# Kernel tuning notes

Hardware: AMD Instinct MI355X
Metric: run time of the kernel (lower is better)

The kernel has to match this reference:

```python
import jax, jax.numpy as jnp
import numpy as np

B, S, D = 8, 2048, 1024
D_FF = 1024  # FeedForward default d_ff
EPS = 1e-5   # nn.LayerNorm default


def layernorm(x, g, b):
    mu = jnp.mean(x, axis=-1, keepdims=True)
    var = jnp.mean(jnp.square(x - mu), axis=-1, keepdims=True)
    return (x - mu) * jax.lax.rsqrt(var + EPS) * g + b


def setup_inputs() -> dict:
    key = jax.random.key(0)
    ks = jax.random.split(key, 12)
    s = 1.0 / np.sqrt(D)
    return {
        "x": jax.random.normal(ks[0], (B, S, D), jnp.float32),
        "mask": jax.random.randint(ks[1], (B, S), 0, 2, jnp.int32),
        "ln1_g": jnp.ones((D,), jnp.float32),
        "ln1_b": jnp.zeros((D,), jnp.float32),
        "Wq": jax.random.normal(ks[2], (D, D), jnp.float32) * s,
        "bq": jnp.zeros((D,), jnp.float32),
        "Wk": jax.random.normal(ks[3], (D, D), jnp.float32) * s,
        "bk": jnp.zeros((D,), jnp.float32),
        "Wo": jax.random.normal(ks[4], (D, D), jnp.float32) * s,
        "bo": jnp.zeros((D,), jnp.float32),
        "ln2_g": jnp.ones((D,), jnp.float32),
        "ln2_b": jnp.zeros((D,), jnp.float32),
        "W1": jax.random.normal(ks[5], (D, D_FF), jnp.float32) * s,
        "b1": jnp.zeros((D_FF,), jnp.float32),
        "W2": jax.random.normal(ks[6], (D_FF, D), jnp.float32) * (1.0 / np.sqrt(D_FF)),
        "b2": jnp.zeros((D,), jnp.float32),
    }


def reference(x, mask, ln1_g, ln1_b, Wq, bq, Wk, bk, Wo, bo, ln2_g, ln2_b, W1, b1, W2, b2):
    # pre-norm
    xn = layernorm(x, ln1_g, ln1_b)
    q = xn @ Wq + bq
    k = xn @ Wk + bk
    v = xn @ Wk + bk  # faithful bug: original uses k_linear for v
    scores = jnp.einsum('bqd,bkd->bqk', q, k) / np.sqrt(D)
    scores = jnp.where(mask[:, None, :] == 0, jnp.float32(-1e9), scores)
    w = jax.nn.softmax(scores, axis=-1)
    attn = jnp.einsum('bqk,bkd->bqd', w, v) @ Wo + bo
    x2 = x + attn  # dropout identity (eval)
    xn2 = layernorm(x2, ln2_g, ln2_b)
    ff = jax.nn.relu(xn2 @ W1 + b1) @ W2 + b2
    out = x2 + ff
    return (out, w)
```

## Files before the change

kernel.cpp:

```cpp
#include <hip/hip_runtime.h>
#include <cstdint>
#include <cstddef>

#define BB 8
#define SS 2048
#define DD 1024

typedef unsigned short bf16_t;
typedef __attribute__((ext_vector_type(8))) short bf16x8;
typedef __attribute__((ext_vector_type(4))) float f32x4;
typedef __attribute__((ext_vector_type(4))) short short4v;

#define EPI_BF16   0
#define EPI_SCORES 1
#define EPI_RESID  2

__device__ __forceinline__ bf16_t f2bf(float f) {
  union { float f; unsigned u; } v; v.f = f;
  unsigned r = v.u + 0x7FFFu + ((v.u >> 16) & 1u);
  return (bf16_t)(r >> 16);
}

__device__ __forceinline__ void async_copy16(const void* g, void* l) {
  auto gp = reinterpret_cast<unsigned int __attribute__((address_space(1)))*>(
      reinterpret_cast<uintptr_t>(g));
  auto lp = reinterpret_cast<unsigned int __attribute__((address_space(3)))*>(
      reinterpret_cast<uintptr_t>(l));
  __builtin_amdgcn_global_load_lds(gp, lp, 16, 0, 0);
}

#define MM(i, j, Af, Bf) \
  acc[i][j] = __builtin_amdgcn_mfma_f32_16x16x32_bf16(Af, Bf, acc[i][j], 0, 0, 0)

#define LDA8(D, MH)                                                        \
  { const char* Ah_ = ldsc + (D) * 65536 + (MH) * 16384;                   \
    aF[0] = *(const bf16x8*)(Ah_ + aro +    0 + s0);                       \
    aF[1] = *(const bf16x8*)(Ah_ + aro + 2048 + s0);                       \
    aF[2] = *(const bf16x8*)(Ah_ + aro + 4096 + s0);                       \
    aF[3] = *(const bf16x8*)(Ah_ + aro + 6144 + s0);                       \
    aF[4] = *(const bf16x8*)(Ah_ + aro +    0 + s1);                       \
    aF[5] = *(const bf16x8*)(Ah_ + aro + 2048 + s1);                       \
    aF[6] = *(const bf16x8*)(Ah_ + aro + 4096 + s1);                       \
    aF[7] = *(const bf16x8*)(Ah_ + aro + 6144 + s1); }

#define LDB4(D, NH, BF)                                                    \
  { const char* Bh_ = ldsc + (D) * 65536 + 32768 + (NH) * 16384;           \
    BF[0] = *(const bf16x8*)(Bh_ + bro +    0 + s0);                       \
    BF[1] = *(const bf16x8*)(Bh_ + bro + 2048 + s0);                       \
    BF[2] = *(const bf16x8*)(Bh_ + bro +    0 + s1);                       \
    BF[3] = *(const bf16x8*)(Bh_ + bro + 2048 + s1); }

#define MFMA16(MH, NH, BF)                                                 \
  __builtin_amdgcn_s_setprio(1);                                           \
  MM((MH)*4+0,(NH)*2+0,aF[0],BF[0]); MM((MH)*4+1,(NH)*2+0,aF[1],BF[0]);    \
  MM((MH)*4+2,(NH)*2+0,aF[2],BF[0]); MM((MH)*4+3,(NH)*2+0,aF[3],BF[0]);    \
  MM((MH)*4+0,(NH)*2+1,aF[0],BF[1]); MM((MH)*4+1,(NH)*2+1,aF[1],BF[1]);    \
  MM((MH)*4+2,(NH)*2+1,aF[2],BF[1]); MM((MH)*4+3,(NH)*2+1,aF[3],BF[1]);    \
  MM((MH)*4+0,(NH)*2+0,aF[4],BF[2]); MM((MH)*4+1,(NH)*2+0,aF[5],BF[2]);    \
  MM((MH)*4+2,(NH)*2+0,aF[6],BF[2]); MM((MH)*4+3,(NH)*2+0,aF[7],BF[2]);    \
  MM((MH)*4+0,(NH)*2+1,aF[4],BF[3]); MM((MH)*4+1,(NH)*2+1,aF[5],BF[3]);    \
  MM((MH)*4+2,(NH)*2+1,aF[6],BF[3]); MM((MH)*4+3,(NH)*2+1,aF[7],BF[3]);    \
  __builtin_amdgcn_s_setprio(0);

template <int EPI, bool RELU>
__global__ __launch_bounds__(512, 2)
void gemm256(const bf16_t* __restrict__ A, const bf16_t* __restrict__ BT,
             void* __restrict__ Cv,
             const float* __restrict__ bias,
             const float* __restrict__ bias2,
             const float* __restrict__ resid,
             const int* __restrict__ mask,
             int Mt, int Nt, int Z, int nchunk,
             int K, int lda, int ldb, int ldc,
             long long sA, long long sB, long long sC, long long sMask,
             float scale)
{
  __shared__ __align__(16) bf16_t lds_[65536];
  char* ldsc = (char*)lds_;

  const int b = blockIdx.x;
  const int Cchunk = (Z * Mt * Nt) >> 3;
  int idx = (b & 7) * Cchunk + (b >> 3);
  const int per_z = Mt * Nt;
  const int z = idx / per_z;  idx -= z * per_z;
  const int per_nc = Mt * nchunk;
  const int nc = idx / per_nc; idx -= nc * per_nc;
  const int mt = idx / nchunk;
  const int nin = idx - mt * nchunk;
  const int m0 = mt * 256;
  const int n0 = (nc * nchunk + nin) * 256;

  const int tid  = threadIdx.x;
  const int wave = tid >> 6;
  const int lane = tid & 63;
  const int wr   = wave >> 2, wc = wave & 3;
  const int lr   = lane & 15, quad = lane >> 4;

  const bf16_t* Ab = A  + (size_t)z * (size_t)sA;
  const bf16_t* Bb = BT + (size_t)z * (size_t)sB;

  f32x4 acc[8][4];
#pragma unroll
  for (int i = 0; i < 8; ++i)
#pragma unroll
    for (int j = 0; j < 4; ++j)
#pragma unroll
      for (int r = 0; r < 4; ++r) acc[i][j][r] = 0.0f;

  const bf16_t* gA[2]; const bf16_t* gB[2]; char* lA[2]; char* lB[2];
#pragma unroll
  for (int u = 0; u < 2; ++u) {
    const int c = tid + u * 512;
    const int rl = c >> 3;
    const int csw = (((c & 7) ^ (rl & 7)) << 3);
    const int rowA = ((rl & 64) << 1) + (rl & 63);
    const int rowB = ((rl & 96) << 1) + (rl & 31);
    gA[u] = Ab + (size_t)(m0 + rowA) * lda + csw;
    gB[u] = Bb + (size_t)(n0 + rowB) * ldb + csw;
    lA[u] = ldsc + c * 16;
    lB[u] = ldsc + 32768 + c * 16;
  }
  const int ldA64 = lda << 6, ldB64 = ldb << 5;

  auto stageA = [&](int d, int mh, int kt) {
    const int go = mh * ldA64 + kt;
    const int lo = d * 65536 + mh * 16384;
#pragma unroll
    for (int u = 0; u < 2; ++u) async_copy16(gA[u] + go, lA[u] + lo);
  };
  auto stageB = [&](int d, int nh, int kt) {
    const int go = nh * ldB64 + kt;
    const int lo = d * 65536 + nh * 16384;
#pragma unroll
    for (int u = 0; u < 2; ++u) async_copy16(gB[u] + go, lB[u] + lo);
  };

  const int s0  = ((quad ^ (lr & 7)) << 4);
  const int s1  = s0 ^ 64;
  const int aro = (wr * 64 + lr) << 7;
  const int bro = (wc * 32 + lr) << 7;

  bf16x8 aF[8];
  bf16x8 bF0[4], bF1[4];

  const int NT = K >> 6;

  stageA(0, 0, 0); stageA(0, 1, 0); stageB(0, 0, 0); stageB(0, 1, 0);
  if (NT > 1) {
    stageA(1, 0, 64); stageB(1, 0, 64);
    asm volatile("s_waitcnt vmcnt(4)" ::: "memory");
  } else {
    asm volatile("s_waitcnt vmcnt(0)" ::: "memory");
  }
  __builtin_amdgcn_s_barrier();

#pragma unroll 2
  for (int t = 0; t < NT; ++t) {
    const int d  = t & 1;
    const int k1 = (t + 1) << 6;
    const int k2 = (t + 2) << 6;

    LDA8(d, 0); LDB4(d, 0, bF0);
    if (t + 1 < NT) stageA(d ^ 1, 1, k1);
    __builtin_amdgcn_s_barrier();
    MFMA16(0, 0, bF0);

    LDB4(d, 1, bF1);
    if (t + 1 < NT) stageB(d ^ 1, 1, k1);
    __builtin_amdgcn_s_barrier();
    MFMA16(0, 1, bF1);

    LDA8(d, 1);
    if (t + 2 < NT) stageA(d, 0, k2);
    __builtin_amdgcn_s_barrier();
    MFMA16(1, 1, bF1);

    if (t + 2 < NT) {
      stageB(d, 0, k2);
      asm volatile("s_waitcnt vmcnt(4)" ::: "memory");
    } else {
      asm volatile("s_waitcnt vmcnt(0)" ::: "memory");
    }
    __builtin_amdgcn_s_barrier();
    MFMA16(1, 0, bF0);
  }

#pragma unroll
  for (int i = 0; i < 8; ++i) {
    const int gmb = m0 + wr * 128 + (i >> 2) * 64 + (i & 3) * 16 + quad * 4;
#pragma unroll
    for (int j = 0; j < 4; ++j) {
      const int gn = n0 + wc * 64 + (j >> 1) * 32 + (j & 1) * 16 + lr;
      float bv = 0.0f;
      if constexpr (EPI != EPI_SCORES) {
        bv = (bias2 && gn >= 1024) ? bias2[gn - 1024] : (bias ? bias[gn] : 0.0f);
      }
#pragma unroll
      for (int r = 0; r < 4; ++r) {
        float v = acc[i][j][r];
        const size_t off = (size_t)z * (size_t)sC + (size_t)(gmb + r) * ldc + gn;
        if constexpr (EPI == EPI_BF16) {
          v += bv;
          if (RELU) v = v > 0.0f ? v : 0.0f;
          ((bf16_t*)Cv)[off] = f2bf(v);
        } else if constexpr (EPI == EPI_SCORES) {
          const int mk = mask[(size_t)z * (size_t)sMask + gn];
          ((float*)Cv)[off] = mk ? v * scale : -1e9f;
        } else {
          ((float*)Cv)[off] = v + bv + resid[(size_t)(gmb + r) * ldc + gn];
        }
      }
    }
  }
}

__global__ __launch_bounds__(256)
void ln_kernel(const float* __restrict__ x, const float* __restrict__ g,
               const float* __restrict__ b, bf16_t* __restrict__ out)
{
  const int row  = blockIdx.x;
  const int t    = threadIdx.x;
  const int wave = t >> 6, lane = t & 63;
  const float4 v = ((const float4*)(x + (size_t)row * DD))[t];

  float s = v.x + v.y + v.z + v.w;
#pragma unroll
  for (int o = 32; o > 0; o >>= 1) s += __shfl_down(s, o);
  __shared__ float red1[4], red2[4];
  if (lane == 0) red1[wave] = s;
  __syncthreads();
  const float mu = (red1[0] + red1[1] + red1[2] + red1[3]) * (1.0f / DD);

  const float d0 = v.x - mu, d1 = v.y - mu, d2 = v.z - mu, d3 = v.w - mu;
  float ss = d0 * d0 + d1 * d1 + d2 * d2 + d3 * d3;
#pragma unroll
  for (int o = 32; o > 0; o >>= 1) ss += __shfl_down(ss, o);
  if (lane == 0) red2[wave] = ss;
  __syncthreads();
  const float var = (red2[0] + red2[1] + red2[2] + red2[3]) * (1.0f / DD);
  const float rs  = rsqrtf(var + 1e-5f);

  const float4 gg = ((const float4*)g)[t];
  const float4 bb = ((const float4*)b)[t];
  short4v o;
  o.x = (short)f2bf(d0 * rs * gg.x + bb.x);
  o.y = (short)f2bf(d1 * rs * gg.y + bb.y);
  o.z = (short)f2bf(d2 * rs * gg.z + bb.z);
  o.w = (short)f2bf(d3 * rs * gg.w + bb.w);
  *(short4v*)(out + (size_t)row * DD + t * 4) = o;
}

__global__ __launch_bounds__(256)
void softmax_kernel(float* __restrict__ w, bf16_t* __restrict__ wb)
{
  const size_t rowoff = (size_t)blockIdx.x * SS;
  float* p = w + rowoff;
  const int t = threadIdx.x;
  const int wave = t >> 6, lane = t & 63;
  float4 v0 = ((float4*)p)[t];
  float4 v1 = ((float4*)p)[t + 256];

  float m = fmaxf(fmaxf(fmaxf(v0.x, v0.y), fmaxf(v0.z, v0.w)),
                  fmaxf(fmaxf(v1.x, v1.y), fmaxf(v1.z, v1.w)));
#pragma unroll
  for (int o = 32; o > 0; o >>= 1) m = fmaxf(m, __shfl_down(m, o));
  __shared__ float red1[4], red2[4];
  if (lane == 0) red1[wave] = m;
  __syncthreads();
  m = fmaxf(fmaxf(red1[0], red1[1]), fmaxf(red1[2], red1[3]));

  v0.x = __expf(v0.x - m); v0.y = __expf(v0.y - m);
  v0.z = __expf(v0.z - m); v0.w = __expf(v0.w - m);
  v1.x = __expf(v1.x - m); v1.y = __expf(v1.y - m);
  v1.z = __expf(v1.z - m); v1.w = __expf(v1.w - m);

  float s = v0.x + v0.y + v0.z + v0.w + v1.x + v1.y + v1.z + v1.w;
#pragma unroll
  for (int o = 32; o > 0; o >>= 1) s += __shfl_down(s, o);
  if (lane == 0) red2[wave] = s;
  __syncthreads();
  const float inv = 1.0f / (red2[0] + red2[1] + red2[2] + red2[3]);

  v0.x *= inv; v0.y *= inv; v0.z *= inv; v0.w *= inv;
  v1.x *= inv; v1.y *= inv; v1.z *= inv; v1.w *= inv;
  ((float4*)p)[t] = v0;
  ((float4*)p)[t + 256] = v1;

  short4v o0 = { (short)f2bf(v0.x), (short)f2bf(v0.y), (short)f2bf(v0.z), (short)f2bf(v0.w) };
  short4v o1 = { (short)f2bf(v1.x), (short)f2bf(v1.y), (short)f2bf(v1.z), (short)f2bf(v1.w) };
  *(short4v*)(wb + rowoff + t * 4)         = o0;
  *(short4v*)(wb + rowoff + (t + 256) * 4) = o1;
}

template <typename ST>
__global__ __launch_bounds__(256)
void transpose_to_bf16(const ST* __restrict__ in, bf16_t* __restrict__ out,
                       int R, int C, int ldin, long long inB, long long outB)
{
  __shared__ float tile[32][33];
  const int tx = threadIdx.x, ty = threadIdx.y;
  const size_t zi = (size_t)blockIdx.z * (size_t)inB;
  const size_t zo = (size_t)blockIdx.z * (size_t)outB;
  const int c0 = blockIdx.x * 32, r0 = blockIdx.y * 32;
#pragma unroll
  for (int k = 0; k < 32; k += 8) {
    ST raw = in[zi + (size_t)(r0 + ty + k) * ldin + (c0 + tx)];
    float v;
    if constexpr (sizeof(ST) == 2) {
      v = __uint_as_float(((unsigned)(unsigned short)raw) << 16);
    } else {
      v = (float)raw;
    }
    tile[ty + k][tx] = v;
  }
  __syncthreads();
#pragma unroll
  for (int k = 0; k < 32; k += 8)
    out[zo + (size_t)(c0 + ty + k) * R + (r0 + tx)] = f2bf(tile[tx][ty + k]);
}

extern "C" void kernel_launch(void* const* d_in, const int* in_sizes, int n_in,
                              void* d_out, int out_size, void* d_ws, size_t ws_size,
                              hipStream_t stream)
{
  const float* x    = (const float*)d_in[0];
  const int*   mask = (const int*)d_in[1];
  const float* ln1g = (const float*)d_in[2];
  const float* ln1b = (const float*)d_in[3];
  const float* Wq   = (const float*)d_in[4];
  const float* bq   = (const float*)d_in[5];
  const float* Wk   = (const float*)d_in[6];
  const float* bk   = (const float*)d_in[7];
  const float* Wo   = (const float*)d_in[8];
  const float* bo   = (const float*)d_in[9];
  const float* ln2g = (const float*)d_in[10];
  const float* ln2b = (const float*)d_in[11];
  const float* W1   = (const float*)d_in[12];
  const float* b1   = (const float*)d_in[13];
  const float* W2   = (const float*)d_in[14];
  const float* b2   = (const float*)d_in[15];

  float* out  = (float*)d_out;
  float* wout = out + (size_t)BB * SS * DD;

  char* ws = (char*)d_ws;
  size_t off = 0;
  auto alloc = [&](size_t bytes) {
    char* p = ws + off; off += (bytes + 255) & ~(size_t)255; return p;
  };
  bf16_t* WqkT = (bf16_t*)alloc((size_t)2 * DD * DD * 2);
  bf16_t* WoT  = (bf16_t*)alloc((size_t)DD * DD * 2);
  bf16_t* W1T  = (bf16_t*)alloc((size_t)DD * DD * 2);
  bf16_t* W2T  = (bf16_t*)alloc((size_t)DD * DD * 2);
  bf16_t* QKb  = (bf16_t*)alloc((size_t)BB * SS * 2 * DD * 2);
  char*   Rwb  = alloc((size_t)64 * 1024 * 1024);
  bf16_t* aV   = (bf16_t*)alloc((size_t)BB * SS * DD * 2);

  bf16_t* wbf = (bf16_t*)Rwb;
  bf16_t* xn2 = (bf16_t*)Rwb;
  bf16_t* h   = (bf16_t*)(Rwb + (size_t)32 * 1024 * 1024);

  bf16_t* xn = (bf16_t*)wout;
  bf16_t* KT = (bf16_t*)out;
  float*  x2 = out;

  const dim3 tb(256);
  const dim3 tg(512);
  const dim3 tt(32, 8);
  const long long SD   = (long long)SS * DD;
  const long long S2   = (long long)SS * SS;
  const long long QKs  = (long long)SS * 2 * DD;

  transpose_to_bf16<float><<<dim3(32, 32, 1), tt, 0, stream>>>(Wq, WqkT, DD, DD, DD, 0, 0);
  transpose_to_bf16<float><<<dim3(32, 32, 1), tt, 0, stream>>>(Wk, WqkT + (size_t)DD * DD, DD, DD, DD, 0, 0);
  transpose_to_bf16<float><<<dim3(32, 32, 1), tt, 0, stream>>>(Wo, WoT, DD, DD, DD, 0, 0);
  transpose_to_bf16<float><<<dim3(32, 32, 1), tt, 0, stream>>>(W1, W1T, DD, DD, DD, 0, 0);
  transpose_to_bf16<float><<<dim3(32, 32, 1), tt, 0, stream>>>(W2, W2T, DD, DD, DD, 0, 0);

  ln_kernel<<<dim3(BB * SS), tb, 0, stream>>>(x, ln1g, ln1b, xn);

  gemm256<EPI_BF16, false><<<dim3(512), tg, 0, stream>>>(
      xn, WqkT, QKb, bq, bk, nullptr, nullptr,
       64, 8, 1, 8,  DD, DD, DD, 2 * DD,
      0, 0, 0, 0, 1.0f);

  gemm256<EPI_SCORES, false><<<dim3(512), tg, 0, stream>>>(
      QKb, QKb + DD, wout, nullptr, nullptr, nullptr, mask,
      8, 8, BB, 8,  DD, 2 * DD, 2 * DD, SS,
      QKs, QKs, S2, SS, 0.03125f);

  softmax_kernel<<<dim3(BB * SS), tb, 0, stream>>>(wout, wbf);

  transpose_to_bf16<bf16_t><<<dim3(32, 64, BB), tt, 0, stream>>>(
      QKb + DD, KT, SS, DD, 2 * DD, QKs, SD);

  gemm256<EPI_BF16, false><<<dim3(256), tg, 0, stream>>>(
      wbf, KT, aV, nullptr, nullptr, nullptr, nullptr,
      8, 4, BB, 4,  SS, SS, SS, DD,
      S2, SD, SD, 0, 1.0f);

  gemm256<EPI_RESID, false><<<dim3(256), tg, 0, stream>>>(
      aV, WoT, x2, bo, nullptr, x, nullptr,
      64, 4, 1, 4, DD, DD, DD, DD, 0, 0, 0, 0, 1.0f);

  ln_kernel<<<dim3(BB * SS), tb, 0, stream>>>(x2, ln2g, ln2b, xn2);

  gemm256<EPI_BF16, true><<<dim3(256), tg, 0, stream>>>(
      xn2, W1T, h, b1, nullptr, nullptr, nullptr,
      64, 4, 1, 4, DD, DD, DD, DD, 0, 0, 0, 0, 1.0f);

  gemm256<EPI_RESID, false><<<dim3(256), tg, 0, stream>>>(
      h, W2T, out, b2, nullptr, x2, nullptr,
      64, 4, 1, 4, DD, DD, DD, DD, 0, 0, 0, 0, 1.0f);
}
```

Measured before the change: 689.8 us.

## Stage bf16 GEMM epilogue through LDS and merge prep/softmax/transpose launches

```diff
diff --git a/kernel.cpp b/kernel.cpp
--- a/kernel.cpp
+++ b/kernel.cpp
@@ -185,59 +185,86 @@
     MFMA16(1, 0, bF0);
   }
 
-#pragma unroll
-  for (int i = 0; i < 8; ++i) {
-    const int gmb = m0 + wr * 128 + (i >> 2) * 64 + (i & 3) * 16 + quad * 4;
-#pragma unroll
-    for (int j = 0; j < 4; ++j) {
-      const int gn = n0 + wc * 64 + (j >> 1) * 32 + (j & 1) * 16 + lr;
-      float bv = 0.0f;
-      if constexpr (EPI != EPI_SCORES) {
-        bv = (bias2 && gn >= 1024) ? bias2[gn - 1024] : (bias ? bias[gn] : 0.0f);
-      }
-#pragma unroll
-      for (int r = 0; r < 4; ++r) {
-        float v = acc[i][j][r];
-        const size_t off = (size_t)z * (size_t)sC + (size_t)(gmb + r) * ldc + gn;
-        if constexpr (EPI == EPI_BF16) {
-          v += bv;
-          if (RELU) v = v > 0.0f ? v : 0.0f;
-          ((bf16_t*)Cv)[off] = f2bf(v);
-        } else if constexpr (EPI == EPI_SCORES) {
-          const int mk = mask[(size_t)z * (size_t)sMask + gn];
-          ((float*)Cv)[off] = mk ? v * scale : -1e9f;
-        } else {
-          ((float*)Cv)[off] = v + bv + resid[(size_t)(gmb + r) * ldc + gn];
+  if constexpr (EPI == EPI_BF16) {
+    char* Wb = ldsc + wave * 16384;
+#pragma unroll
+    for (int i = 0; i < 8; ++i) {
+      const int mb = (i >> 2) * 64 + (i & 3) * 16 + quad * 4;
+#pragma unroll
+      for (int j = 0; j < 4; ++j) {
+        const int nl = (j >> 1) * 32 + (j & 1) * 16 + lr;
+        const int gn = n0 + wc * 64 + nl;
+        const float bv = (bias2 && gn >= 1024) ? bias2[gn - 1024]
+                       : (bias ? bias[gn] : 0.0f);
+#pragma unroll
+        for (int r = 0; r < 4; ++r) {
+          float v = acc[i][j][r] + bv;
+          if (RELU) v = fmaxf(v, 0.0f);
+          const int m = mb + r;
+          const int nb = nl * 2;
+          const int phys = (m << 7) + (((nb & ~15) ^ ((m & 7) << 4)) | (nb & 15));
+          *(bf16_t*)(Wb + phys) = f2bf(v);
         }
       }
     }
-  }
-}
-
-__global__ __launch_bounds__(256)
-void ln_kernel(const float* __restrict__ x, const float* __restrict__ g,
-               const float* __restrict__ b, bf16_t* __restrict__ out)
-{
-  const int row  = blockIdx.x;
-  const int t    = threadIdx.x;
+    asm volatile("s_waitcnt lgkmcnt(0)" ::: "memory");
+    bf16_t* Cb = (bf16_t*)Cv + (size_t)z * (size_t)sC
+               + (size_t)(m0 + wr * 128) * ldc + (n0 + wc * 64);
+#pragma unroll
+    for (int p = 0; p < 16; ++p) {
+      const int m = p * 8 + (lane >> 3);
+      const int c = lane & 7;
+      const bf16x8 vv = *(const bf16x8*)(Wb + (m << 7) + (((c ^ (m & 7)) << 4)));
+      *(bf16x8*)(Cb + (size_t)m * ldc + c * 8) = vv;
+    }
+  } else {
+#pragma unroll
+    for (int i = 0; i < 8; ++i) {
+      const int gmb = m0 + wr * 128 + (i >> 2) * 64 + (i & 3) * 16 + quad * 4;
+#pragma unroll
+      for (int j = 0; j < 4; ++j) {
+        const int gn = n0 + wc * 64 + (j >> 1) * 32 + (j & 1) * 16 + lr;
+        float bv = 0.0f;
+        if constexpr (EPI == EPI_RESID) { bv = bias ? bias[gn] : 0.0f; }
+#pragma unroll
+        for (int r = 0; r < 4; ++r) {
+          float v = acc[i][j][r];
+          const size_t off = (size_t)z * (size_t)sC + (size_t)(gmb + r) * ldc + gn;
+          if constexpr (EPI == EPI_SCORES) {
+            const int mk = mask[(size_t)z * (size_t)sMask + gn];
+            ((float*)Cv)[off] = mk ? v * scale : -1e9f;
+          } else {
+            ((float*)Cv)[off] = v + bv + resid[(size_t)(gmb + r) * ldc + gn];
+          }
+        }
+      }
+    }
+  }
+}
+
+__device__ __forceinline__ void ln_body(const float* __restrict__ x,
+                                        const float* __restrict__ g,
+                                        const float* __restrict__ b,
+                                        bf16_t* __restrict__ out,
+                                        int row, int t, float* red)
+{
   const int wave = t >> 6, lane = t & 63;
   const float4 v = ((const float4*)(x + (size_t)row * DD))[t];
 
   float s = v.x + v.y + v.z + v.w;
 #pragma unroll
   for (int o = 32; o > 0; o >>= 1) s += __shfl_down(s, o);
-  __shared__ float red1[4], red2[4];
-  if (lane == 0) red1[wave] = s;
+  if (lane == 0) red[wave] = s;
   __syncthreads();
-  const float mu = (red1[0] + red1[1] + red1[2] + red1[3]) * (1.0f / DD);
+  const float mu = (red[0] + red[1] + red[2] + red[3]) * (1.0f / DD);
 
   const float d0 = v.x - mu, d1 = v.y - mu, d2 = v.z - mu, d3 = v.w - mu;
   float ss = d0 * d0 + d1 * d1 + d2 * d2 + d3 * d3;
 #pragma unroll
   for (int o = 32; o > 0; o >>= 1) ss += __shfl_down(ss, o);
-  if (lane == 0) red2[wave] = ss;
+  if (lane == 0) red[4 + wave] = ss;
   __syncthreads();
-  const float var = (red2[0] + red2[1] + red2[2] + red2[3]) * (1.0f / DD);
+  const float var = (red[4] + red[5] + red[6] + red[7]) * (1.0f / DD);
   const float rs  = rsqrtf(var + 1e-5f);
 
   const float4 gg = ((const float4*)g)[t];
@@ -250,12 +277,12 @@
   *(short4v*)(out + (size_t)row * DD + t * 4) = o;
 }
 
-__global__ __launch_bounds__(256)
-void softmax_kernel(float* __restrict__ w, bf16_t* __restrict__ wb)
-{
-  const size_t rowoff = (size_t)blockIdx.x * SS;
+__device__ __forceinline__ void softmax_body(float* __restrict__ w,
+                                             bf16_t* __restrict__ wb,
+                                             int row, int t, float* red)
+{
+  const size_t rowoff = (size_t)row * SS;
   float* p = w + rowoff;
-  const int t = threadIdx.x;
   const int wave = t >> 6, lane = t & 63;
   float4 v0 = ((float4*)p)[t];
   float4 v1 = ((float4*)p)[t + 256];
@@ -264,10 +291,9 @@
                   fmaxf(fmaxf(v1.x, v1.y), fmaxf(v1.z, v1.w)));
 #pragma unroll
   for (int o = 32; o > 0; o >>= 1) m = fmaxf(m, __shfl_down(m, o));
-  __shared__ float red1[4], red2[4];
-  if (lane == 0) red1[wave] = m;
+  if (lane == 0) red[wave] = m;
   __syncthreads();
-  m = fmaxf(fmaxf(red1[0], red1[1]), fmaxf(red1[2], red1[3]));
+  m = fmaxf(fmaxf(red[0], red[1]), fmaxf(red[2], red[3]));
 
   v0.x = __expf(v0.x - m); v0.y = __expf(v0.y - m);
   v0.z = __expf(v0.z - m); v0.w = __expf(v0.w - m);
@@ -277,9 +303,9 @@
   float s = v0.x + v0.y + v0.z + v0.w + v1.x + v1.y + v1.z + v1.w;
 #pragma unroll
   for (int o = 32; o > 0; o >>= 1) s += __shfl_down(s, o);
-  if (lane == 0) red2[wave] = s;
+  if (lane == 0) red[4 + wave] = s;
   __syncthreads();
-  const float inv = 1.0f / (red2[0] + red2[1] + red2[2] + red2[3]);
+  const float inv = 1.0f / (red[4] + red[5] + red[6] + red[7]);
 
   v0.x *= inv; v0.y *= inv; v0.z *= inv; v0.w *= inv;
   v1.x *= inv; v1.y *= inv; v1.z *= inv; v1.w *= inv;
@@ -293,15 +319,16 @@
 }
 
 template <typename ST>
-__global__ __launch_bounds__(256)
-void transpose_to_bf16(const ST* __restrict__ in, bf16_t* __restrict__ out,
-                       int R, int C, int ldin, long long inB, long long outB)
-{
-  __shared__ float tile[32][33];
-  const int tx = threadIdx.x, ty = threadIdx.y;
-  const size_t zi = (size_t)blockIdx.z * (size_t)inB;
-  const size_t zo = (size_t)blockIdx.z * (size_t)outB;
-  const int c0 = blockIdx.x * 32, r0 = blockIdx.y * 32;
+__device__ __forceinline__ void transpose_body(const ST* __restrict__ in,
+                                               bf16_t* __restrict__ out,
+                                               int R, int ldin,
+                                               long long inB, long long outB,
+                                               int xb, int yb, int zb,
+                                               int tx, int ty, float* tile)
+{
+  const size_t zi = (size_t)zb * (size_t)inB;
+  const size_t zo = (size_t)zb * (size_t)outB;
+  const int c0 = xb * 32, r0 = yb * 32;
 #pragma unroll
   for (int k = 0; k < 32; k += 8) {
     ST raw = in[zi + (size_t)(r0 + ty + k) * ldin + (c0 + tx)];
@@ -311,12 +338,63 @@
     } else {
       v = (float)raw;
     }
-    tile[ty + k][tx] = v;
+    tile[(ty + k) * 33 + tx] = v;
   }
   __syncthreads();
 #pragma unroll
   for (int k = 0; k < 32; k += 8)
-    out[zo + (size_t)(c0 + ty + k) * R + (r0 + tx)] = f2bf(tile[tx][ty + k]);
+    out[zo + (size_t)(c0 + ty + k) * R + (r0 + tx)] = f2bf(tile[tx * 33 + ty + k]);
+}
+
+__global__ __launch_bounds__(256)
+void prep_kernel(const float* __restrict__ Wq, const float* __restrict__ Wk,
+                 const float* __restrict__ Wo, const float* __restrict__ W1,
+                 const float* __restrict__ W2,
+                 bf16_t* __restrict__ WqkT, bf16_t* __restrict__ WoT,
+                 bf16_t* __restrict__ W1T, bf16_t* __restrict__ W2T,
+                 const float* __restrict__ x, const float* __restrict__ g,
+                 const float* __restrict__ b, bf16_t* __restrict__ xn)
+{
+  __shared__ float smem[32 * 33];
+  const int bid = blockIdx.x;
+  const int tid = threadIdx.x;
+  if (bid < 5120) {
+    const int wi = bid >> 10;
+    const int rem = bid & 1023;
+    const float* src = wi == 0 ? Wq : wi == 1 ? Wk : wi == 2 ? Wo : wi == 3 ? W1 : W2;
+    bf16_t* dst = wi == 0 ? WqkT : wi == 1 ? (WqkT + (size_t)DD * DD)
+                 : wi == 2 ? WoT : wi == 3 ? W1T : W2T;
+    transpose_body<float>(src, dst, DD, DD, 0, 0,
+                          rem & 31, rem >> 5, 0, tid & 31, tid >> 5, smem);
+  } else {
+    ln_body(x, g, b, xn, bid - 5120, tid, smem);
+  }
+}
+
+__global__ __launch_bounds__(256)
+void softkt_kernel(float* __restrict__ w, bf16_t* __restrict__ wb,
+                   const bf16_t* __restrict__ qkb_k, bf16_t* __restrict__ KT)
+{
+  __shared__ float smem[32 * 33];
+  const int bid = blockIdx.x;
+  const int tid = threadIdx.x;
+  if (bid < BB * SS) {
+    softmax_body(w, wb, bid, tid, smem);
+  } else {
+    const int t2 = bid - BB * SS;
+    const int zb = t2 >> 11, rem = t2 & 2047;
+    transpose_body<bf16_t>(qkb_k, KT, SS, 2 * DD,
+                           (long long)SS * 2 * DD, (long long)SS * DD,
+                           rem & 31, rem >> 5, zb, tid & 31, tid >> 5, smem);
+  }
+}
+
+__global__ __launch_bounds__(256)
+void ln_kernel(const float* __restrict__ x, const float* __restrict__ g,
+               const float* __restrict__ b, bf16_t* __restrict__ out)
+{
+  __shared__ float red[8];
+  ln_body(x, g, b, out, blockIdx.x, threadIdx.x, red);
 }
 
 extern "C" void kernel_launch(void* const* d_in, const int* in_sizes, int n_in,
@@ -366,18 +444,12 @@
 
   const dim3 tb(256);
   const dim3 tg(512);
-  const dim3 tt(32, 8);
   const long long SD   = (long long)SS * DD;
   const long long S2   = (long long)SS * SS;
   const long long QKs  = (long long)SS * 2 * DD;
 
-  transpose_to_bf16<float><<<dim3(32, 32, 1), tt, 0, stream>>>(Wq, WqkT, DD, DD, DD, 0, 0);
-  transpose_to_bf16<float><<<dim3(32, 32, 1), tt, 0, stream>>>(Wk, WqkT + (size_t)DD * DD, DD, DD, DD, 0, 0);
-  transpose_to_bf16<float><<<dim3(32, 32, 1), tt, 0, stream>>>(Wo, WoT, DD, DD, DD, 0, 0);
-  transpose_to_bf16<float><<<dim3(32, 32, 1), tt, 0, stream>>>(W1, W1T, DD, DD, DD, 0, 0);
-  transpose_to_bf16<float><<<dim3(32, 32, 1), tt, 0, stream>>>(W2, W2T, DD, DD, DD, 0, 0);
-
-  ln_kernel<<<dim3(BB * SS), tb, 0, stream>>>(x, ln1g, ln1b, xn);
+  prep_kernel<<<dim3(5120 + BB * SS), tb, 0, stream>>>(
+      Wq, Wk, Wo, W1, W2, WqkT, WoT, W1T, W2T, x, ln1g, ln1b, xn);
 
   gemm256<EPI_BF16, false><<<dim3(512), tg, 0, stream>>>(
       xn, WqkT, QKb, bq, bk, nullptr, nullptr,
@@ -389,10 +461,7 @@
       8, 8, BB, 8,  DD, 2 * DD, 2 * DD, SS,
       QKs, QKs, S2, SS, 0.03125f);
 
-  softmax_kernel<<<dim3(BB * SS), tb, 0, stream>>>(wout, wbf);
-
-  transpose_to_bf16<bf16_t><<<dim3(32, 64, BB), tt, 0, stream>>>(
-      QKb + DD, KT, SS, DD, 2 * DD, QKs, SD);
+  softkt_kernel<<<dim3(2 * BB * SS), tb, 0, stream>>>(wout, wbf, QKb + DD, KT);
 
   gemm256<EPI_BF16, false><<<dim3(256), tg, 0, stream>>>(
       wbf, KT, aV, nullptr, nullptr, nullptr, nullptr,
```

After: 686.2 us. About the same (-0.5%).
